# Optimization experiments

Hardware: AMD Instinct MI355X
Metric: run time of the kernel (lower is better)

Reference implementation:

```python
import jax, jax.numpy as jnp
import numpy as np

N_QUBITS = 12
N_LAYERS = 4
BATCH = 4096
DIM = 2 ** N_QUBITS  # 4096


def _apply_1q(state, U, q):
    """Apply 2x2 complex gate U to qubit q. state: (B,) + (2,)*n, wire 0 = MSB (axis q+1)."""
    state = jnp.moveaxis(state, q + 1, -1)
    state = state @ U.T
    return jnp.moveaxis(state, -1, q + 1)


def _apply_cnot(state, c, t):
    """CNOT with control c, target t: flip target amplitudes where control bit == 1."""
    flipped = jnp.flip(state, axis=t + 1)
    shape = [2 if i == c + 1 else 1 for i in range(state.ndim)]
    ctrl = jnp.arange(2).reshape(shape)
    return jnp.where(ctrl == 1, flipped, state)


def setup_inputs() -> dict:
    key = jax.random.key(0)
    k1, k2 = jax.random.split(key)
    x = jax.random.normal(k1, (BATCH, DIM), dtype=jnp.float32)
    weights = jax.random.normal(k2, (N_LAYERS, N_QUBITS, 2), dtype=jnp.float32) * 0.1
    return {"x": x, "weights": weights}


def reference(x, weights):
    n, L = N_QUBITS, N_LAYERS
    B = x.shape[0]
    # AmplitudeEmbedding with normalize=True
    norm = jnp.linalg.norm(x, axis=-1, keepdims=True)
    state = (x / norm).astype(jnp.complex64).reshape((B,) + (2,) * n)
    for layer in range(L):
        for q in range(n):
            ty = weights[layer, q, 0]
            tz = weights[layer, q, 1]
            c, s = jnp.cos(ty / 2), jnp.sin(ty / 2)
            em = jnp.exp(-0.5j * tz.astype(jnp.complex64))  # e^{-i tz/2}
            ep = jnp.exp(+0.5j * tz.astype(jnp.complex64))
            # U = RZ(tz) @ RY(ty), fused single 2x2 gate per qubit
            U = jnp.stack([
                jnp.stack([c * em, -s * em]),
                jnp.stack([s * ep, c * ep]),
            ]).astype(jnp.complex64)
            state = _apply_1q(state, U, q)
        for q in range(n - 1):
            state = _apply_cnot(state, q, q + 1)
        if n > 2:
            state = _apply_cnot(state, n - 1, 0)
    probs = jnp.abs(state) ** 2  # (B,) + (2,)*n, float32
    reduce_axes = tuple(range(1, probs.ndim))
    outs = []
    for q in range(n):
        shape = [2 if i == q + 1 else 1 for i in range(probs.ndim)]
        sign = jnp.array([1.0, -1.0], dtype=probs.dtype).reshape(shape)
        outs.append(jnp.sum(probs * sign, axis=reduce_axes))
    return jnp.stack(outs, axis=-1)  # (B, n_qubits) <Z_q> expvals
```

## Files before the change

### kernel.cpp

```cpp
#include <hip/hip_runtime.h>

#define NQ   12
#define DIM  4096
#define NL   4
#define BLK  256

typedef unsigned short u16;
typedef unsigned int   u32;

struct L12 { u16 b[NQ]; };

static constexpr u32 lap(const L12& A, u32 x){ u32 r=0; for(int p=0;p<NQ;++p) if((x>>p)&1u) r^=A.b[p]; return r; }
static constexpr L12 lcomp(const L12& A, const L12& B){ L12 r{}; for(int p=0;p<NQ;++p) r.b[p]=(u16)lap(A,(u32)B.b[p]); return r; }
static constexpr L12 lident(){ L12 r{}; for(int p=0;p<NQ;++p) r.b[p]=(u16)(1u<<p); return r; }

static constexpr u32 applyT(u32 i){
  i ^= ((i>>0)&1u) << 11;
  for(int q=10;q>=0;--q){ int pc=11-q, pt=10-q; i ^= ((i>>pc)&1u) << pt; }
  return i;
}
static constexpr L12 lT(){ L12 t{}; for(int p=0;p<NQ;++p) t.b[p]=(u16)applyT(1u<<p); return t; }

static constexpr L12 linv(const L12& A){
  u16 v[NQ]; u16 u[NQ];
  for(int p=0;p<NQ;++p){ v[p]=A.b[p]; u[p]=(u16)(1u<<p); }
  for(int t=0;t<NQ;++t){
    int p=t; while(!((v[p]>>t)&1u)) ++p;
    u16 tv=v[p]; v[p]=v[t]; v[t]=tv; u16 tu=u[p]; u[p]=u[t]; u[t]=tu;
    for(int k=0;k<NQ;++k) if(k!=t && ((v[k]>>t)&1u)){ v[k]^=v[t]; u[k]^=u[t]; }
  }
  L12 r{}; for(int p=0;p<NQ;++p) r.b[p]=u[p]; return r;
}
static constexpr L12 ltr(const L12& A){
  L12 r{}; for(int p=0;p<NQ;++p) for(int q=0;q<NQ;++q) if((A.b[p]>>q)&1u) r.b[q]=(u16)(r.b[q]|(1u<<p));
  return r;
}
static constexpr int cpop(u32 v){ int n=0; while(v){ n+=(int)(v&1u); v>>=1; } return n; }

struct Tables {
  u16 cm[12][16];
  u16 wg[12][4];
  u16 sp[12][4];
  u16 wexp[NQ];
};

static constexpr Tables make_tables(){
  Tables tb{};
  const L12 T   = lT();
  const L12 Tit = ltr(linv(T));
  L12 A = lident();
  L12 W = lident();
  for(int l=0;l<NL;++l){
    for(int g=0;g<3;++g){
      const int st = l*3+g;
      u16 mm[4]={0,0,0,0};
      for(int i=0;i<4;++i){ mm[i]=A.b[4*g+i]; tb.wg[st][i]=W.b[4*g+i]; }
      u32 ech[4]={0,0,0,0}; int piv[4]={0,0,0,0};
      for(int i=0;i<4;++i){
        u32 v=mm[i];
        for(int k=0;k<i;++k) if((v>>piv[k])&1u) v^=ech[k];
        int t2=11; while(!((v>>t2)&1u)) --t2;
        piv[i]=t2; ech[i]=v;
      }
      for(int a2=0;a2<4;++a2) for(int b2=a2+1;b2<4;++b2)
        if(piv[b2]<piv[a2]){ int tt=piv[a2]; piv[a2]=piv[b2]; piv[b2]=tt; }
      for(int i=0;i<4;++i) tb.sp[st][i]=(u16)piv[i];
      for(int c=0;c<16;++c){ u32 m=0; for(int i=0;i<4;++i) if((c>>i)&1) m^=mm[i]; tb.cm[st][c]=(u16)m; }
    }
    A = lcomp(A, T);
    W = lcomp(W, Tit);
  }
  for(int p=0;p<NQ;++p) tb.wexp[p]=W.b[p];
  return tb;
}

__device__ constexpr Tables TB = make_tables();

static constexpr u16 UIMG[12] = {1,2,4,8, 3,5,6,7, 9,10,11,13};

static constexpr u32 swz(u32 j){
  u32 f=0;
  for(int k=4;k<12;++k) if((j>>k)&1u) f ^= (u32)UIMG[k];
  return j ^ (f & 15u);
}

struct Derived {
  u32 lane_c[12][8];
  u32 smb[12][4];
  u32 scmb[12][16];
  u32 g0lane[8];
  u32 u11lane[8];
  u32 u11smb[4];
  u16 csgn[12];
  u16 pm[12];
};

static constexpr Derived make_derived(){
  const Tables tb = make_tables();
  Derived d{};
  for(int st=0; st<12; ++st){
    bool isp[12]={false,false,false,false,false,false,false,false,false,false,false,false};
    for(int i=0;i<4;++i) isp[tb.sp[st][i]]=true;
    int np[8]; int nn=0;
    for(int p=0;p<12;++p) if(!isp[p]) np[nn++]=p;
    int best=-1;
    for(int ms=0; ms<256; ++ms){
      int pc=0; for(int k=0;k<8;++k) pc+=(ms>>k)&1;
      if(pc!=6) continue;
      u16 bas[4]={0,0,0,0}; int r=0;
      for(int k=0;k<8;++k){
        if(!((ms>>k)&1)) continue;
        u16 x=(u16)(UIMG[np[k]]&15);
        while(x){
          int hb=3; while(!((x>>hb)&1)) --hb;
          if(bas[hb]) x=(u16)(x^bas[hb]);
          else { bas[hb]=x; ++r; x=0; }
        }
      }
      if(r==4){ best=ms; break; }
    }
    if(best<0) best=0x3F;
    int pos[8]; int lo=0, hi=6;
    for(int k=0;k<8;++k){ if((best>>k)&1) pos[lo++]=np[k]; else pos[hi++]=np[k]; }
    for(int k=0;k<8;++k){
      const u32 addr = swz(1u<<pos[k])<<3;
      u32 nib=0;
      for(int i=0;i<4;++i) nib |= (u32)((tb.wg[st][i]>>pos[k])&1u)<<i;
      d.lane_c[st][k] = addr | (nib<<28);
      if(st==0)  d.g0lane[k]  = 1u<<pos[k];
      if(st==11) d.u11lane[k] = 1u<<pos[k];
    }
    for(int i=0;i<4;++i)  d.smb[st][i]  = swz((u32)tb.cm[st][1<<i])<<3;
    for(int c=0;c<16;++c) d.scmb[st][c] = swz((u32)tb.cm[st][c])<<3;
    if(st==11) for(int i=0;i<4;++i) d.u11smb[i] = (u32)tb.cm[11][1<<i];
  }
  for(int q=0;q<12;++q){
    d.pm[q] = tb.wexp[11-q];
    u16 m=0;
    for(int c=0;c<16;++c){
      const int par = cpop((u32)tb.cm[11][c] & (u32)tb.wexp[11-q]) & 1;
      m |= (u16)(par<<c);
    }
    d.csgn[q]=m;
  }
  return d;
}

__device__ constexpr Derived DV = make_derived();

template<int ST, bool WITHW>
__device__ __forceinline__ void gates(float (&ar)[16], float (&ai)[16], const float4* __restrict__ gw){
#pragma unroll
  for(int i=0;i<4;++i){
    const float4 g = gw[ST*4+i];
#pragma unroll
    for(int c=0;c<16;++c){
      if((c>>i)&1) continue;
      const int c1 = c|(1<<i);
      float ur = fmaf(-g.x, ar[c1], ar[c]);
      float ui = fmaf(-g.x, ai[c1], ai[c]);
      float vr = fmaf( g.y, ur, ar[c1]);
      float vi = fmaf( g.y, ui, ai[c1]);
      ar[c] = fmaf(-g.x, vr, ur);
      ai[c] = fmaf(-g.x, vi, ui);
      if(WITHW){
        const float t = fmaf(-g.z, vi, vr);
        vi = fmaf( g.w, t, vi);
        vr = fmaf(-g.z, vi, t);
      }
      ar[c1]=vr; ai[c1]=vi;
    }
  }
}

template<int ST, bool WITHW>
__device__ __forceinline__ void mid_step(const u32* msk, char* lds, const float4* __restrict__ gw){
  u32 acc=0;
#pragma unroll
  for(int k=0;k<8;++k) acc ^= DV.lane_c[ST][k]&msk[k];
  const u32 nib = acc>>28;
  u32 base = acc & 0x0FFFFFFFu;
#pragma unroll
  for(int i=0;i<4;++i) base ^= DV.smb[ST][i] & (0u-((nib>>i)&1u));
  u32 ad[16]; float ar[16], ai[16];
#pragma unroll
  for(int c=0;c<16;++c){
    ad[c] = base ^ DV.scmb[ST][c];
    const float2 v = *(const float2*)(lds+ad[c]);
    ar[c]=v.x; ai[c]=v.y;
  }
  gates<ST,WITHW>(ar,ai,gw);
#pragma unroll
  for(int c=0;c<16;++c){ float2 v; v.x=ar[c]; v.y=ai[c]; *(float2*)(lds+ad[c])=v; }
  __syncthreads();
}

__global__ void prep_kernel(const float* __restrict__ w, float4* __restrict__ gw){
  const int t = threadIdx.x;
  if(t < NL*NQ){
    const int l=t/NQ, p=t%NQ, q=(NQ-1)-p;
    const float ty=w[(l*NQ+q)*2+0], tz=w[(l*NQ+q)*2+1];
    gw[t]=make_float4(tanf(0.25f*ty), sinf(0.5f*ty), tanf(0.5f*tz), sinf(tz));
  }
}

__global__ __launch_bounds__(BLK, 4) void qsim_kernel(const float* __restrict__ x,
                                                      const float4* __restrict__ gw,
                                                      float* __restrict__ out)
{
  __shared__ float2 st2[DIM];
  __shared__ float  wred[4][13];
  char* lds = (char*)st2;
  const int tid = threadIdx.x;
  const int bb  = blockIdx.x;

  u32 msk[8];
#pragma unroll
  for(int k=0;k<8;++k) msk[k]=0u-((u32)(tid>>k)&1u);

  u32 rep0=0, acc0=0;
#pragma unroll
  for(int k=0;k<8;++k){ rep0 ^= DV.g0lane[k]&msk[k]; acc0 ^= DV.lane_c[0][k]&msk[k]; }
  const u32 base0 = acc0 & 0x0FFFFFFFu;

  float ar[16], ai[16];
  const float* xr = x + (size_t)bb*DIM + rep0;
#pragma unroll
  for(int s=0;s<4;++s){
    const float4 v = *reinterpret_cast<const float4*>(xr + 4*s);
    ar[4*s+0]=v.x; ar[4*s+1]=v.y; ar[4*s+2]=v.z; ar[4*s+3]=v.w;
    ai[4*s+0]=0.f; ai[4*s+1]=0.f; ai[4*s+2]=0.f; ai[4*s+3]=0.f;
  }
  gates<0,true>(ar,ai,gw);
#pragma unroll
  for(int c=0;c<16;++c){ float2 v; v.x=ar[c]; v.y=ai[c];
    *(float2*)(lds + (base0 ^ DV.scmb[0][c])) = v; }
  __syncthreads();

  mid_step<1,true >(msk,lds,gw);
  mid_step<2,true >(msk,lds,gw);
  mid_step<3,true >(msk,lds,gw);
  mid_step<4,true >(msk,lds,gw);
  mid_step<5,true >(msk,lds,gw);
  mid_step<6,true >(msk,lds,gw);
  mid_step<7,true >(msk,lds,gw);
  mid_step<8,true >(msk,lds,gw);
  mid_step<9,false>(msk,lds,gw);
  mid_step<10,false>(msk,lds,gw);

  {
    u32 acc=0, urep=0;
#pragma unroll
    for(int k=0;k<8;++k){ acc ^= DV.lane_c[11][k]&msk[k]; urep ^= DV.u11lane[k]&msk[k]; }
    const u32 nib = acc>>28;
    u32 base = acc & 0x0FFFFFFFu;
#pragma unroll
    for(int i=0;i<4;++i){ const u32 mi=0u-((nib>>i)&1u); base ^= DV.smb[11][i]&mi; urep ^= DV.u11smb[i]&mi; }
#pragma unroll
    for(int c=0;c<16;++c){
      const float2 v = *(const float2*)(lds + (base ^ DV.scmb[11][c]));
      ar[c]=v.x; ai[c]=v.y;
    }
    gates<11,false>(ar,ai,gw);

    float pr[16]; float nrm=0.f;
#pragma unroll
    for(int c=0;c<16;++c) pr[c]=fmaf(ar[c],ar[c], ai[c]*ai[c]);
#pragma unroll
    for(int c=0;c<16;++c) nrm += pr[c];
    float accq[12];
#pragma unroll
    for(int q=0;q<12;++q){
      float a=0.f;
#pragma unroll
      for(int c=0;c<16;++c){ if((DV.csgn[q]>>c)&1) a-=pr[c]; else a+=pr[c]; }
      const u32 sb = ((u32)__popc(urep & (u32)DV.pm[q]) & 1u)<<31;
      accq[q]=__uint_as_float(__float_as_uint(a)^sb);
    }
#pragma unroll
    for(int o=32;o;o>>=1){
      nrm += __shfl_xor(nrm,o);
#pragma unroll
      for(int q=0;q<12;++q) accq[q]+=__shfl_xor(accq[q],o);
    }
    const int wid=tid>>6;
    if((tid&63)==0){
#pragma unroll
      for(int q=0;q<12;++q) wred[wid][q]=accq[q];
      wred[wid][12]=nrm;
    }
    __syncthreads();
    if(tid<NQ){
      const float s0=wred[0][tid]+wred[1][tid]+wred[2][tid]+wred[3][tid];
      const float sn=wred[0][12]+wred[1][12]+wred[2][12]+wred[3][12];
      out[(size_t)bb*NQ+tid]=s0/sn;
    }
  }
}

extern "C" void kernel_launch(void* const* d_in, const int* in_sizes, int n_in,
                              void* d_out, int out_size, void* d_ws, size_t ws_size,
                              hipStream_t stream) {
  const float* x = (const float*)d_in[0];
  const float* w = (const float*)d_in[1];
  float* out = (float*)d_out;
  float4* gw = (float4*)d_ws;
  const int B = in_sizes[0] / DIM;
  prep_kernel<<<1, 64, 0, stream>>>(w, gw);
  qsim_kernel<<<B, BLK, 0, stream>>>(x, gw, out);
}
```

Baseline: 112.7 us.

## Pair gate stages so each thread owns its slice across barriers, dropping syncs

```diff
diff --git a/kernel.cpp b/kernel.cpp
--- a/kernel.cpp
+++ b/kernel.cpp
@@ -35,12 +35,10 @@
   L12 r{}; for(int p=0;p<NQ;++p) for(int q=0;q<NQ;++q) if((A.b[p]>>q)&1u) r.b[q]=(u16)(r.b[q]|(1u<<p));
   return r;
 }
-static constexpr int cpop(u32 v){ int n=0; while(v){ n+=(int)(v&1u); v>>=1; } return n; }
 
 struct Tables {
   u16 cm[12][16];
   u16 wg[12][4];
-  u16 sp[12][4];
   u16 wexp[NQ];
 };
 
@@ -55,16 +53,6 @@
       const int st = l*3+g;
       u16 mm[4]={0,0,0,0};
       for(int i=0;i<4;++i){ mm[i]=A.b[4*g+i]; tb.wg[st][i]=W.b[4*g+i]; }
-      u32 ech[4]={0,0,0,0}; int piv[4]={0,0,0,0};
-      for(int i=0;i<4;++i){
-        u32 v=mm[i];
-        for(int k=0;k<i;++k) if((v>>piv[k])&1u) v^=ech[k];
-        int t2=11; while(!((v>>t2)&1u)) --t2;
-        piv[i]=t2; ech[i]=v;
-      }
-      for(int a2=0;a2<4;++a2) for(int b2=a2+1;b2<4;++b2)
-        if(piv[b2]<piv[a2]){ int tt=piv[a2]; piv[a2]=piv[b2]; piv[b2]=tt; }
-      for(int i=0;i<4;++i) tb.sp[st][i]=(u16)piv[i];
       for(int c=0;c<16;++c){ u32 m=0; for(int i=0;i<4;++i) if((c>>i)&1) m^=mm[i]; tb.cm[st][c]=(u16)m; }
     }
     A = lcomp(A, T);
@@ -74,15 +62,127 @@
   return tb;
 }
 
-__device__ constexpr Tables TB = make_tables();
-
 static constexpr u16 UIMG[12] = {1,2,4,8, 3,5,6,7, 9,10,11,13};
-
 static constexpr u32 swz(u32 j){
   u32 f=0;
   for(int k=4;k<12;++k) if((j>>k)&1u) f ^= (u32)UIMG[k];
   return j ^ (f & 15u);
 }
+
+static constexpr int par16(u16 v){ int n=0; for(int i=0;i<12;++i) n ^= (int)((v>>i)&1u); return n; }
+
+struct Ech { u16 s[12]; };
+static constexpr u16 ered(const Ech& e, u16 x){
+  for(int it=0; it<13 && x; ++it){
+    int lb=0; for(int b=0;b<12;++b) if((x>>b)&1u) lb=b;
+    if(e.s[lb]) x=(u16)(x^e.s[lb]); else break;
+  }
+  return x;
+}
+static constexpr bool eadd(Ech& e, u16 x){
+  x=ered(e,x); if(!x) return false;
+  int lb=0; for(int b=0;b<12;++b) if((x>>b)&1u) lb=b;
+  e.s[lb]=x; return true;
+}
+
+struct NullB { u16 v[12]; int n; };
+static constexpr NullB nullspace(const u16* rows, int m){
+  u16 rr[12]={}; int pc[12]={}; int nr=0;
+  for(int i=0;i<m;++i){
+    u16 x=rows[i];
+    for(int j=0;j<nr;++j) if((x>>pc[j])&1u) x=(u16)(x^rr[j]);
+    if(!x) continue;
+    int lb=0; for(int b=0;b<12;++b) if((x>>b)&1u) lb=b;
+    for(int j=0;j<nr;++j) if((rr[j]>>lb)&1u) rr[j]=(u16)(rr[j]^x);
+    rr[nr]=x; pc[nr]=lb; ++nr;
+  }
+  NullB nb{};
+  for(int f=0;f<12;++f){
+    bool isp=false; for(int j=0;j<nr;++j) if(pc[j]==f) isp=true;
+    if(isp) continue;
+    u16 x=(u16)(1u<<f);
+    for(int j=0;j<nr;++j) if((rr[j]>>f)&1u) x=(u16)(x|(1u<<pc[j]));
+    nb.v[nb.n++]=x;
+  }
+  return nb;
+}
+
+static constexpr void pickN(const NullB& K, const u16* seed, int nseed, bool lowclear, u16* out, int n){
+  Ech e{}; for(int i=0;i<nseed;++i) eadd(e, seed[i]);
+  Ech bank{};
+  for(int p=0;p<n;++p){
+    u16 best=0; int bg=-1;
+    for(int i=0;i<K.n;++i){
+      u16 c=K.v[i]; if(lowclear) c=(u16)(c&0xFF0u); if(!c) continue;
+      if(!ered(e,c)) continue;
+      u16 img=(u16)(swz(c)&15u);
+      int g=(img && ered(bank,img))?1:0;
+      if(g>bg){ bg=g; best=c; }
+      if(bg==1) break;
+    }
+    if(bg<1){
+      for(int i=0;i<K.n && bg<1;++i) for(int j=i+1;j<K.n && bg<1;++j){
+        u16 c=(u16)(K.v[i]^K.v[j]); if(lowclear) c=(u16)(c&0xFF0u); if(!c) continue;
+        if(!ered(e,c)) continue;
+        u16 img=(u16)(swz(c)&15u);
+        int g=(img && ered(bank,img))?1:0;
+        if(g>bg){ bg=g; best=c; }
+      }
+    }
+    out[p]=best;
+    if(best){ eadd(e,best); u16 img=(u16)(swz(best)&15u); if(img) eadd(bank,img); }
+  }
+}
+
+struct PairB { u16 rva[8]; u16 rvb[8]; bool ok; };
+
+static constexpr PairB make_pair_basis(int a){
+  const Tables tb = make_tables();
+  const int b=a+1;
+  u16 A[4], B[4], AB[8];
+  for(int i=0;i<4;++i){ A[i]=tb.cm[a][1u<<i]; B[i]=tb.cm[b][1u<<i]; AB[i]=A[i]; AB[4+i]=B[i]; }
+  PairB r{}; r.ok=true;
+  NullB ann = nullspace(AB,8);
+  if(ann.n<2) r.ok=false;
+  u16 f6 = r.ok?ann.v[0]:(u16)1, f7 = r.ok?ann.v[1]:(u16)2;
+  u16 fr[2]={f6,f7};
+  NullB K = nullspace(fr,2);
+  const bool lc = (a==0);
+  u16 v6=0, v7=0;
+  for(u32 j=1;j<4096u && !(v6&&v7); ++j){
+    u16 x=(u16)j; if(lc) x=(u16)(x&0xFF0u); if(!x) continue;
+    int s6=par16((u16)(x&f6)), s7=par16((u16)(x&f7));
+    if(s6==1&&s7==0&&v6==0) v6=x;
+    else if(s6==0&&s7==1&&v7==0) v7=x;
+  }
+  if(!v6||!v7) r.ok=false;
+  pickN(K, A, 4, lc,    r.rva, 6);
+  pickN(K, B, 4, false, r.rvb, 6);
+  r.rva[6]=v6; r.rva[7]=v7; r.rvb[6]=v6; r.rvb[7]=v7;
+  if(r.ok){
+    Ech ea{}; for(int i=0;i<4;++i) eadd(ea,A[i]);
+    for(int k=0;k<6;++k){ if(!r.rva[k] || !eadd(ea,r.rva[k])) r.ok=false; }
+    for(int i=0;i<4;++i) if(ered(ea,B[i])) r.ok=false;
+    if(!eadd(ea,v6)) r.ok=false;
+    if(!eadd(ea,v7)) r.ok=false;
+    Ech eb{}; for(int i=0;i<4;++i) eadd(eb,B[i]);
+    for(int k=0;k<8;++k){ if(!r.rvb[k] || !eadd(eb,r.rvb[k])) r.ok=false; }
+    if(lc) for(int k=0;k<8;++k) if(r.rva[k]&15u) r.ok=false;
+  }
+  if(!r.ok){
+    NullB full{}; full.n=12; for(int i=0;i<12;++i) full.v[i]=(u16)(1u<<i);
+    pickN(full, A, 4, lc,    r.rva, 8);
+    pickN(full, B, 4, false, r.rvb, 8);
+  }
+  return r;
+}
+
+static constexpr PairB PB0 = make_pair_basis(0);
+static constexpr PairB PB1 = make_pair_basis(2);
+static constexpr PairB PB2 = make_pair_basis(4);
+static constexpr PairB PB3 = make_pair_basis(6);
+static constexpr PairB PB4 = make_pair_basis(8);
+static constexpr PairB PB5 = make_pair_basis(10);
 
 struct Derived {
   u32 lane_c[12][8];
@@ -91,62 +191,46 @@
   u32 g0lane[8];
   u32 u11lane[8];
   u32 u11smb[4];
-  u16 csgn[12];
   u16 pm[12];
+  u16 mu[12];
+  bool freeb[12];
 };
 
-static constexpr Derived make_derived(){
+static constexpr Derived make_derived(const PairB& p0,const PairB& p1,const PairB& p2,
+                                      const PairB& p3,const PairB& p4,const PairB& p5){
   const Tables tb = make_tables();
+  const PairB pb[6] = {p0,p1,p2,p3,p4,p5};
   Derived d{};
   for(int st=0; st<12; ++st){
-    bool isp[12]={false,false,false,false,false,false,false,false,false,false,false,false};
-    for(int i=0;i<4;++i) isp[tb.sp[st][i]]=true;
-    int np[8]; int nn=0;
-    for(int p=0;p<12;++p) if(!isp[p]) np[nn++]=p;
-    int best=-1;
-    for(int ms=0; ms<256; ++ms){
-      int pc=0; for(int k=0;k<8;++k) pc+=(ms>>k)&1;
-      if(pc!=6) continue;
-      u16 bas[4]={0,0,0,0}; int r=0;
-      for(int k=0;k<8;++k){
-        if(!((ms>>k)&1)) continue;
-        u16 x=(u16)(UIMG[np[k]]&15);
-        while(x){
-          int hb=3; while(!((x>>hb)&1)) --hb;
-          if(bas[hb]) x=(u16)(x^bas[hb]);
-          else { bas[hb]=x; ++r; x=0; }
-        }
-      }
-      if(r==4){ best=ms; break; }
-    }
-    if(best<0) best=0x3F;
-    int pos[8]; int lo=0, hi=6;
-    for(int k=0;k<8;++k){ if((best>>k)&1) pos[lo++]=np[k]; else pos[hi++]=np[k]; }
+    const PairB& P = pb[st/2];
+    const u16* rv = (st%2==0)?P.rva:P.rvb;
     for(int k=0;k<8;++k){
-      const u32 addr = swz(1u<<pos[k])<<3;
       u32 nib=0;
-      for(int i=0;i<4;++i) nib |= (u32)((tb.wg[st][i]>>pos[k])&1u)<<i;
-      d.lane_c[st][k] = addr | (nib<<28);
-      if(st==0)  d.g0lane[k]  = 1u<<pos[k];
-      if(st==11) d.u11lane[k] = 1u<<pos[k];
-    }
-    for(int i=0;i<4;++i)  d.smb[st][i]  = swz((u32)tb.cm[st][1<<i])<<3;
+      for(int i=0;i<4;++i) nib |= (u32)(par16((u16)(rv[k]&tb.wg[st][i]))&1)<<i;
+      d.lane_c[st][k] = (swz((u32)rv[k])<<3) | (nib<<28);
+      if(st==0)  d.g0lane[k]=(u32)rv[k];
+      if(st==11) d.u11lane[k]=(u32)rv[k];
+    }
+    for(int i=0;i<4;++i)  d.smb[st][i]  = swz((u32)tb.cm[st][1u<<i])<<3;
     for(int c=0;c<16;++c) d.scmb[st][c] = swz((u32)tb.cm[st][c])<<3;
-    if(st==11) for(int i=0;i<4;++i) d.u11smb[i] = (u32)tb.cm[11][1<<i];
+    if(st==11) for(int i=0;i<4;++i) d.u11smb[i]=(u32)tb.cm[11][1u<<i];
+    d.freeb[st] = (st%2==0) ? pb[st/2].ok : false;
   }
   for(int q=0;q<12;++q){
-    d.pm[q] = tb.wexp[11-q];
-    u16 m=0;
-    for(int c=0;c<16;++c){
-      const int par = cpop((u32)tb.cm[11][c] & (u32)tb.wexp[11-q]) & 1;
-      m |= (u16)(par<<c);
-    }
-    d.csgn[q]=m;
+    d.pm[q]=tb.wexp[11-q];
+    u32 m=0;
+    for(int i=0;i<4;++i) m |= (u32)(par16((u16)(tb.cm[11][1u<<i]&tb.wexp[11-q]))&1)<<i;
+    d.mu[q]=(u16)m;
   }
   return d;
 }
 
-__device__ constexpr Derived DV = make_derived();
+static constexpr Derived DVH = make_derived(PB0,PB1,PB2,PB3,PB4,PB5);
+__device__ constexpr Derived DV = DVH;
+
+__device__ __forceinline__ void fence_free(){
+  asm volatile("s_waitcnt lgkmcnt(0)" ::: "memory");
+}
 
 template<int ST, bool WITHW>
 __device__ __forceinline__ void gates(float (&ar)[16], float (&ai)[16], const float4* __restrict__ gw){
@@ -192,7 +276,11 @@
   gates<ST,WITHW>(ar,ai,gw);
 #pragma unroll
   for(int c=0;c<16;++c){ float2 v; v.x=ar[c]; v.y=ai[c]; *(float2*)(lds+ad[c])=v; }
-  __syncthreads();
+}
+
+template<int ST>
+__device__ __forceinline__ void boundary(){
+  if constexpr (DVH.freeb[ST]) fence_free(); else __syncthreads();
 }
 
 __global__ void prep_kernel(const float* __restrict__ w, float4* __restrict__ gw){
@@ -204,12 +292,11 @@
   }
 }
 
-__global__ __launch_bounds__(BLK, 4) void qsim_kernel(const float* __restrict__ x,
+__global__ __launch_bounds__(BLK, 5) void qsim_kernel(const float* __restrict__ x,
                                                       const float4* __restrict__ gw,
                                                       float* __restrict__ out)
 {
   __shared__ float2 st2[DIM];
-  __shared__ float  wred[4][13];
   char* lds = (char*)st2;
   const int tid = threadIdx.x;
   const int bb  = blockIdx.x;
@@ -235,18 +322,18 @@
 #pragma unroll
   for(int c=0;c<16;++c){ float2 v; v.x=ar[c]; v.y=ai[c];
     *(float2*)(lds + (base0 ^ DV.scmb[0][c])) = v; }
-  __syncthreads();
-
-  mid_step<1,true >(msk,lds,gw);
-  mid_step<2,true >(msk,lds,gw);
-  mid_step<3,true >(msk,lds,gw);
-  mid_step<4,true >(msk,lds,gw);
-  mid_step<5,true >(msk,lds,gw);
-  mid_step<6,true >(msk,lds,gw);
-  mid_step<7,true >(msk,lds,gw);
-  mid_step<8,true >(msk,lds,gw);
-  mid_step<9,false>(msk,lds,gw);
-  mid_step<10,false>(msk,lds,gw);
+  boundary<0>();
+
+  mid_step<1,true >(msk,lds,gw); boundary<1>();
+  mid_step<2,true >(msk,lds,gw); boundary<2>();
+  mid_step<3,true >(msk,lds,gw); boundary<3>();
+  mid_step<4,true >(msk,lds,gw); boundary<4>();
+  mid_step<5,true >(msk,lds,gw); boundary<5>();
+  mid_step<6,true >(msk,lds,gw); boundary<6>();
+  mid_step<7,true >(msk,lds,gw); boundary<7>();
+  mid_step<8,true >(msk,lds,gw); boundary<8>();
+  mid_step<9,false>(msk,lds,gw); boundary<9>();
+  mid_step<10,false>(msk,lds,gw); boundary<10>();
 
   {
     u32 acc=0, urep=0;
@@ -263,36 +350,44 @@
     }
     gates<11,false>(ar,ai,gw);
 
-    float pr[16]; float nrm=0.f;
+    float pr[16];
 #pragma unroll
     for(int c=0;c<16;++c) pr[c]=fmaf(ar[c],ar[c], ai[c]*ai[c]);
 #pragma unroll
-    for(int c=0;c<16;++c) nrm += pr[c];
+    for(int b=1;b<16;b<<=1){
+#pragma unroll
+      for(int c=0;c<16;++c){
+        if(c&b) continue;
+        const float u=pr[c], v=pr[c|b];
+        pr[c]=u+v; pr[c|b]=u-v;
+      }
+    }
+    const float nrm = pr[0];
     float accq[12];
 #pragma unroll
     for(int q=0;q<12;++q){
-      float a=0.f;
-#pragma unroll
-      for(int c=0;c<16;++c){ if((DV.csgn[q]>>c)&1) a-=pr[c]; else a+=pr[c]; }
       const u32 sb = ((u32)__popc(urep & (u32)DV.pm[q]) & 1u)<<31;
-      accq[q]=__uint_as_float(__float_as_uint(a)^sb);
-    }
+      accq[q]=__uint_as_float(__float_as_uint(pr[DV.mu[q]])^sb);
+    }
+    float nrm2 = nrm;
 #pragma unroll
     for(int o=32;o;o>>=1){
-      nrm += __shfl_xor(nrm,o);
+      nrm2 += __shfl_xor(nrm2,o);
 #pragma unroll
       for(int q=0;q<12;++q) accq[q]+=__shfl_xor(accq[q],o);
     }
+    __syncthreads();
+    float* wredf = (float*)lds;
     const int wid=tid>>6;
     if((tid&63)==0){
 #pragma unroll
-      for(int q=0;q<12;++q) wred[wid][q]=accq[q];
-      wred[wid][12]=nrm;
+      for(int q=0;q<12;++q) wredf[wid*13+q]=accq[q];
+      wredf[wid*13+12]=nrm2;
     }
     __syncthreads();
     if(tid<NQ){
-      const float s0=wred[0][tid]+wred[1][tid]+wred[2][tid]+wred[3][tid];
-      const float sn=wred[0][12]+wred[1][12]+wred[2][12]+wred[3][12];
+      const float s0=wredf[0*13+tid]+wredf[1*13+tid]+wredf[2*13+tid]+wredf[3*13+tid];
+      const float sn=wredf[0*13+12]+wredf[1*13+12]+wredf[2*13+12]+wredf[3*13+12];
       out[(size_t)bb*NQ+tid]=s0/sn;
     }
   }
```

Result: slower. 117.4 us (+4.1%).
